# Kernel tuning notes

Measured on AMD Instinct MI355X. Metric: run time of the kernel, lower is better.

The kernel has to match this reference:

```python
import jax, jax.numpy as jnp
import numpy as np

N, E = 40000, 640000
DIN, C, EDIM = 128, 128, 32  # heads=1, out_channels=128

def setup_inputs() -> dict:
    key = jax.random.key(0)
    ks = jax.random.split(key, 9)
    x = jax.random.normal(ks[0], (N, DIN), dtype=jnp.float32)
    edge_index = jax.random.randint(ks[1], (2, E), 0, N, dtype=jnp.int64)
    edge_attr = jax.random.normal(ks[2], (E, EDIM), dtype=jnp.float32)
    s = 1.0 / np.sqrt(DIN)
    W = jax.random.normal(ks[3], (DIN, C), dtype=jnp.float32) * s
    W_edge = jax.random.normal(ks[4], (EDIM, C), dtype=jnp.float32) / np.sqrt(EDIM)
    att_src = jax.random.normal(ks[5], (C,), dtype=jnp.float32) * s
    att_dst = jax.random.normal(ks[6], (C,), dtype=jnp.float32) * s
    att_edge = jax.random.normal(ks[7], (C,), dtype=jnp.float32) * s
    bias = jnp.zeros((C,), dtype=jnp.float32)
    return {"x": x, "edge_index": edge_index, "edge_attr": edge_attr,
            "W": W, "W_edge": W_edge, "att_src": att_src, "att_dst": att_dst,
            "att_edge": att_edge, "bias": bias}

def reference(x, edge_index, edge_attr, W, W_edge, att_src, att_dst, att_edge, bias):
    # GATConv (heads=1) with edge features
    h = x @ W                      # [N, C] transformed node features
    a_src = h @ att_src            # [N] per-node source attention logits
    a_dst = h @ att_dst            # [N]
    src, dst = edge_index[0], edge_index[1]
    e = edge_attr @ W_edge         # [E, C]
    a_edge = e @ att_edge          # [E]
    alpha = a_src[src] + a_dst[dst] + a_edge            # [E]
    alpha = jax.nn.leaky_relu(alpha, negative_slope=0.2)
    # segment softmax over incoming edges of each destination node
    amax = jax.ops.segment_max(alpha, dst, num_segments=N)
    amax = jnp.where(jnp.isfinite(amax), amax, 0.0)     # empty segments -> -inf guard
    ex = jnp.exp(alpha - amax[dst])
    denom = jax.ops.segment_sum(ex, dst, num_segments=N)
    w = ex / (denom[dst] + 1e-16)                       # PyG softmax epsilon
    out = jax.ops.segment_sum(h[src] * w[:, None], dst, num_segments=N)  # [N, C]
    return out + bias
```

## Files before the change

kernel.cpp:

```cpp
#include <hip/hip_runtime.h>
#include <hip/hip_bf16.h>
#include <hip/hip_fp16.h>


#define DIN 128
#define CCH 128
#define EDIM 32
#define XS_LD 68

__device__ __forceinline__ unsigned pack_bf2(float a, float b) {
    __hip_bfloat16 x = __float2bfloat16(a);
    __hip_bfloat16 y = __float2bfloat16(b);
    unsigned short ux = *(unsigned short*)&x;
    unsigned short uy = *(unsigned short*)&y;
    return (unsigned)ux | ((unsigned)uy << 16);
}

__global__ __launch_bounds__(256) void gemm_h(
    const float* __restrict__ x, const float* __restrict__ W,
    const float* __restrict__ att_src, const float* __restrict__ att_dst,
    const int* __restrict__ ei, unsigned* __restrict__ hb,
    float* __restrict__ a_src, float* __restrict__ a_dst,
    int* __restrict__ count, int N, int E) {
    __shared__ float xs[64 * XS_LD];
    __shared__ float wl[64 * CCH];
    const int t = threadIdx.x;
    const int tx = t & 15;
    const int ty = t >> 4;
    const int row0 = blockIdx.x * 64;

    {
        const int* eid = ei + E;
        const int stride = gridDim.x * 256;
        for (int e = blockIdx.x * 256 + t; e < E; e += stride)
            atomicAdd(&count[eid[e]], 1);
    }

    float acc[4][8];
#pragma unroll
    for (int r = 0; r < 4; ++r)
#pragma unroll
        for (int c = 0; c < 8; ++c) acc[r][c] = 0.0f;

    for (int kh = 0; kh < 2; ++kh) {
        __syncthreads();
        {
            const float4* xg = (const float4*)x;
#pragma unroll
            for (int i = 0; i < 4; ++i) {
                int j4 = t + 256 * i;
                int r = j4 >> 4;
                int k = (j4 & 15) * 4;
                float4 v = xg[(size_t)(row0 + r) * 32 + kh * 16 + (j4 & 15)];
                *(float4*)&xs[r * XS_LD + k] = v;
            }
        }
        {
            const float4* wg = (const float4*)W;
#pragma unroll
            for (int i = 0; i < 8; ++i) {
                int j4 = t + 256 * i;
                int k = j4 >> 5;
                int c4 = j4 & 31;
                float4 v = wg[(size_t)(kh * 64 + k) * 32 + c4];
                *(float4*)&wl[k * CCH + c4 * 4] = v;
            }
        }
        __syncthreads();

#pragma unroll 4
        for (int k4 = 0; k4 < 64; k4 += 4) {
            float xr[4][4];
#pragma unroll
            for (int r = 0; r < 4; ++r) {
                float4 v = *(const float4*)&xs[(ty * 4 + r) * XS_LD + k4];
                xr[r][0] = v.x; xr[r][1] = v.y; xr[r][2] = v.z; xr[r][3] = v.w;
            }
            float wr[4][8];
#pragma unroll
            for (int i = 0; i < 4; ++i) {
                float4 w0 = *(const float4*)&wl[(k4 + i) * CCH + tx * 8];
                float4 w1 = *(const float4*)&wl[(k4 + i) * CCH + tx * 8 + 4];
                wr[i][0] = w0.x; wr[i][1] = w0.y; wr[i][2] = w0.z; wr[i][3] = w0.w;
                wr[i][4] = w1.x; wr[i][5] = w1.y; wr[i][6] = w1.z; wr[i][7] = w1.w;
            }
#pragma unroll
            for (int i = 0; i < 4; ++i)
#pragma unroll
                for (int r = 0; r < 4; ++r)
#pragma unroll
                    for (int c = 0; c < 8; ++c)
                        acc[r][c] += xr[r][i] * wr[i][c];
        }
    }

    float asv[8], adv[8];
#pragma unroll
    for (int c = 0; c < 8; ++c) {
        asv[c] = att_src[tx * 8 + c];
        adv[c] = att_dst[tx * 8 + c];
    }
#pragma unroll
    for (int r = 0; r < 4; ++r) {
        const int row = row0 + ty * 4 + r;
        unsigned u0 = pack_bf2(acc[r][0], acc[r][1]);
        unsigned u1 = pack_bf2(acc[r][2], acc[r][3]);
        unsigned u2 = pack_bf2(acc[r][4], acc[r][5]);
        unsigned u3 = pack_bf2(acc[r][6], acc[r][7]);
        *(uint4*)&hb[(size_t)row * 64 + tx * 4] = make_uint4(u0, u1, u2, u3);
        float ps = 0.0f, pd = 0.0f;
#pragma unroll
        for (int c = 0; c < 8; ++c) {
            ps += acc[r][c] * asv[c];
            pd += acc[r][c] * adv[c];
        }
        ps += __shfl_down(ps, 8, 16);
        pd += __shfl_down(pd, 8, 16);
        ps += __shfl_down(ps, 4, 16);
        pd += __shfl_down(pd, 4, 16);
        ps += __shfl_down(ps, 2, 16);
        pd += __shfl_down(pd, 2, 16);
        ps += __shfl_down(ps, 1, 16);
        pd += __shfl_down(pd, 1, 16);
        if (tx == 0) {
            a_src[row] = ps;
            a_dst[row] = pd;
        }
    }
}

__global__ __launch_bounds__(256) void scan_part(const int* __restrict__ count,
                                                 int* __restrict__ bsum, int N4) {
    int i4 = blockIdx.x * 256 + threadIdx.x;
    int s = 0;
    if (i4 < N4) {
        int4 vv = ((const int4*)count)[i4];
        s = vv.x + vv.y + vv.z + vv.w;
    }
#pragma unroll
    for (int off = 32; off; off >>= 1) s += __shfl_down(s, off);
    __shared__ int wsum[4];
    if ((threadIdx.x & 63) == 0) wsum[threadIdx.x >> 6] = s;
    __syncthreads();
    if (threadIdx.x == 0)
        bsum[blockIdx.x] = wsum[0] + wsum[1] + wsum[2] + wsum[3];
}

__global__ __launch_bounds__(256) void scan_apply(const int* __restrict__ count,
                                                  const int* __restrict__ bsum,
                                                  int* __restrict__ cursor,
                                                  int N4) {
    __shared__ int s_boff;
    __shared__ int wt[4];
    if (threadIdx.x == 0) {
        int s = 0;
        for (int i = 0; i < (int)blockIdx.x; ++i) s += bsum[i];
        s_boff = s;
    }
    int i4 = blockIdx.x * 256 + threadIdx.x;
    int4 vv = make_int4(0, 0, 0, 0);
    if (i4 < N4) vv = ((const int4*)count)[i4];
    int s = vv.x + vv.y + vv.z + vv.w;
    int lane = threadIdx.x & 63, w = threadIdx.x >> 6;
    int inc = s;
#pragma unroll
    for (int off = 1; off < 64; off <<= 1) {
        int u = __shfl_up(inc, off);
        if (lane >= off) inc += u;
    }
    if (lane == 63) wt[w] = inc;
    __syncthreads();
    int woff = 0;
    for (int i = 0; i < w; ++i) woff += wt[i];
    int exd = s_boff + woff + inc - s;
    if (i4 < N4) {
        int4 o;
        o.x = exd;
        o.y = exd + vv.x;
        o.z = exd + vv.x + vv.y;
        o.w = exd + vv.x + vv.y + vv.z;
        ((int4*)cursor)[i4] = o;
    }
}

__global__ __launch_bounds__(256) void edge_fill(
    const int* __restrict__ ei, const float* __restrict__ ea,
    const float* __restrict__ W_edge, const float* __restrict__ att_edge,
    const float* __restrict__ a_src, const float* __restrict__ a_dst,
    int* __restrict__ cursor, unsigned* __restrict__ pairs, int E) {
    __shared__ float vpart[8][EDIM];
    __shared__ float vl[EDIM];
    const int t = threadIdx.x;
    {
        int j = t & 31, seg = t >> 5;
        const float* wr = W_edge + j * CCH + seg * 16;
        const float* ar = att_edge + seg * 16;
        float p = 0.0f;
#pragma unroll
        for (int k = 0; k < 16; ++k) p += wr[k] * ar[k];
        vpart[seg][j] = p;
    }
    __syncthreads();
    if (t < EDIM) {
        float s = 0.0f;
#pragma unroll
        for (int i = 0; i < 8; ++i) s += vpart[i][t];
        vl[t] = s;
    }
    __syncthreads();

    int e = blockIdx.x * 256 + t;
    if (e >= E) return;
    const float4* ea4 = (const float4*)(ea + (size_t)e * EDIM);
    float s = 0.0f;
#pragma unroll
    for (int j = 0; j < 8; ++j) {
        float4 q = ea4[j];
        s += q.x * vl[4 * j] + q.y * vl[4 * j + 1] + q.z * vl[4 * j + 2] +
             q.w * vl[4 * j + 3];
    }
    int sn = ei[e];
    int dn = ei[E + e];
    float alpha = a_src[sn] + a_dst[dn] + s;
    alpha = alpha > 0.0f ? alpha : 0.2f * alpha;
    float ex = __expf(alpha);
    unsigned rec = (unsigned)(unsigned short)sn |
                   ((unsigned)__half_as_ushort(__float2half(ex)) << 16);
    int p = atomicAdd(&cursor[dn], 1);
    pairs[p] = rec;
}

#define GATHER_EDGE(rec)                                                      \
    {                                                                         \
        unsigned q = hb[(size_t)((rec) & 0xffffu) * 64 + lane];               \
        float exv = __half2float(__ushort_as_half((unsigned short)((rec) >> 16))); \
        a0 += exv * __uint_as_float(q << 16);                                 \
        a1 += exv * __uint_as_float(q & 0xffff0000u);                         \
        sum += exv;                                                           \
    }

__global__ __launch_bounds__(256) void gather_k(
    const int* __restrict__ count, const int* __restrict__ cursor,
    const unsigned* __restrict__ pairs, const unsigned* __restrict__ hb,
    const float* __restrict__ bias, float* __restrict__ out, int N) {
    int n = blockIdx.x * 4 + (threadIdx.x >> 6);
    int lane = threadIdx.x & 63;
    if (n >= N) return;
    int cnt = count[n];
    int start = cursor[n] - cnt;
    float a0 = 0.0f, a1 = 0.0f, sum = 0.0f;
    int j = 0;
    int head = (4 - (start & 3)) & 3;
    if (head > cnt) head = cnt;
    for (; j < head; ++j) {
        unsigned r = pairs[start + j];
        GATHER_EDGE(r);
    }
    int nq = (cnt - j) >> 2;
    if (nq > 0) {
        const uint4* pp4 = (const uint4*)(pairs + start + j);
        uint4 cur = pp4[0];
        for (int g = 0; g + 1 < nq; ++g) {
            uint4 nxt = pp4[g + 1];
            unsigned q0 = hb[(size_t)(cur.x & 0xffffu) * 64 + lane];
            unsigned q1 = hb[(size_t)(cur.y & 0xffffu) * 64 + lane];
            unsigned q2 = hb[(size_t)(cur.z & 0xffffu) * 64 + lane];
            unsigned q3 = hb[(size_t)(cur.w & 0xffffu) * 64 + lane];
            float e0 = __half2float(__ushort_as_half((unsigned short)(cur.x >> 16)));
            float e1 = __half2float(__ushort_as_half((unsigned short)(cur.y >> 16)));
            float e2 = __half2float(__ushort_as_half((unsigned short)(cur.z >> 16)));
            float e3 = __half2float(__ushort_as_half((unsigned short)(cur.w >> 16)));
            a0 += e0 * __uint_as_float(q0 << 16);
            a1 += e0 * __uint_as_float(q0 & 0xffff0000u);
            a0 += e1 * __uint_as_float(q1 << 16);
            a1 += e1 * __uint_as_float(q1 & 0xffff0000u);
            a0 += e2 * __uint_as_float(q2 << 16);
            a1 += e2 * __uint_as_float(q2 & 0xffff0000u);
            a0 += e3 * __uint_as_float(q3 << 16);
            a1 += e3 * __uint_as_float(q3 & 0xffff0000u);
            sum += (e0 + e1) + (e2 + e3);
            cur = nxt;
        }
        {
            unsigned q0 = hb[(size_t)(cur.x & 0xffffu) * 64 + lane];
            unsigned q1 = hb[(size_t)(cur.y & 0xffffu) * 64 + lane];
            unsigned q2 = hb[(size_t)(cur.z & 0xffffu) * 64 + lane];
            unsigned q3 = hb[(size_t)(cur.w & 0xffffu) * 64 + lane];
            float e0 = __half2float(__ushort_as_half((unsigned short)(cur.x >> 16)));
            float e1 = __half2float(__ushort_as_half((unsigned short)(cur.y >> 16)));
            float e2 = __half2float(__ushort_as_half((unsigned short)(cur.z >> 16)));
            float e3 = __half2float(__ushort_as_half((unsigned short)(cur.w >> 16)));
            a0 += e0 * __uint_as_float(q0 << 16);
            a1 += e0 * __uint_as_float(q0 & 0xffff0000u);
            a0 += e1 * __uint_as_float(q1 << 16);
            a1 += e1 * __uint_as_float(q1 & 0xffff0000u);
            a0 += e2 * __uint_as_float(q2 << 16);
            a1 += e2 * __uint_as_float(q2 & 0xffff0000u);
            a0 += e3 * __uint_as_float(q3 << 16);
            a1 += e3 * __uint_as_float(q3 & 0xffff0000u);
            sum += (e0 + e1) + (e2 + e3);
        }
        j += nq * 4;
    }
    for (; j < cnt; ++j) {
        unsigned r = pairs[start + j];
        GATHER_EDGE(r);
    }
    float inv = 1.0f / (sum + 1e-16f);
    float2 bv = *(const float2*)&bias[2 * lane];
    float2 o;
    o.x = a0 * inv + bv.x;
    o.y = a1 * inv + bv.y;
    *(float2*)&out[(size_t)n * CCH + 2 * lane] = o;
}

extern "C" void kernel_launch(void* const* d_in, const int* in_sizes, int n_in,
                              void* d_out, int out_size, void* d_ws, size_t ws_size,
                              hipStream_t stream) {
    const float* x        = (const float*)d_in[0];
    const int*   ei       = (const int*)d_in[1];
    const float* ea       = (const float*)d_in[2];
    const float* W        = (const float*)d_in[3];
    const float* W_edge   = (const float*)d_in[4];
    const float* att_src  = (const float*)d_in[5];
    const float* att_dst  = (const float*)d_in[6];
    const float* att_edge = (const float*)d_in[7];
    const float* bias     = (const float*)d_in[8];
    float* out = (float*)d_out;

    const int N = in_sizes[0] / DIN;
    const int E = in_sizes[2] / EDIM;
    const int N4 = N / 4;
    const int NB = (N4 + 255) / 256;

    char* ws = (char*)d_ws;
    unsigned* hb     = (unsigned*)ws;
    unsigned* pairs  = (unsigned*)(ws + (size_t)N * 64 * 4);
    float*    a_src  = (float*)(pairs + E);
    float*    a_dst  = a_src + N;
    int*      count  = (int*)(a_dst + N);
    int*      cursor = count + N;
    int*      bsum   = cursor + N;

    hipMemsetAsync(count, 0, (size_t)N * sizeof(int), stream);

    gemm_h<<<N / 64, 256, 0, stream>>>(x, W, att_src, att_dst, ei, hb,
                                       a_src, a_dst, count, N, E);
    scan_part<<<NB, 256, 0, stream>>>(count, bsum, N4);
    scan_apply<<<NB, 256, 0, stream>>>(count, bsum, cursor, N4);
    edge_fill<<<(E + 255) / 256, 256, 0, stream>>>(ei, ea, W_edge, att_edge,
                                                   a_src, a_dst, cursor, pairs, E);
    gather_k<<<(N + 3) / 4, 256, 0, stream>>>(count, cursor, pairs, hb, bias, out, N);
}
```

Before: 260.6 us.

## Record per-edge rank during counting to remove atomic cursor in edge fill

The counting atomics in gemm_h now return each edge's rank within its destination bucket, stored as a 16-bit value. edge_fill computes its output slot as offset plus rank instead of issuing a second atomicAdd on a cursor. a_dst and the offset are packed into one float2 per node so a single gather serves both. edge_fill also handles four edges per thread so independent loads can overlap. The cost is an extra E-sized rank write and read, and a rank that overflows if any in-degree exceeds 65535.

```diff
diff --git a/kernel.cpp b/kernel.cpp
--- a/kernel.cpp
+++ b/kernel.cpp
@@ -21,7 +21,8 @@
     const float* __restrict__ att_src, const float* __restrict__ att_dst,
     const int* __restrict__ ei, unsigned* __restrict__ hb,
     float* __restrict__ a_src, float* __restrict__ a_dst,
-    int* __restrict__ count, int N, int E) {
+    int* __restrict__ count, unsigned short* __restrict__ rank,
+    int N, int E) {
     __shared__ float xs[64 * XS_LD];
     __shared__ float wl[64 * CCH];
     const int t = threadIdx.x;
@@ -32,8 +33,10 @@
     {
         const int* eid = ei + E;
         const int stride = gridDim.x * 256;
-        for (int e = blockIdx.x * 256 + t; e < E; e += stride)
-            atomicAdd(&count[eid[e]], 1);
+        for (int e = blockIdx.x * 256 + t; e < E; e += stride) {
+            int r = atomicAdd(&count[eid[e]], 1);
+            rank[e] = (unsigned short)r;
+        }
     }
 
     float acc[4][8];
@@ -146,10 +149,10 @@
         bsum[blockIdx.x] = wsum[0] + wsum[1] + wsum[2] + wsum[3];
 }
 
-__global__ __launch_bounds__(256) void scan_apply(const int* __restrict__ count,
-                                                  const int* __restrict__ bsum,
-                                                  int* __restrict__ cursor,
-                                                  int N4) {
+__global__ __launch_bounds__(256) void scan_apply(
+    const int* __restrict__ count, const int* __restrict__ bsum,
+    const float* __restrict__ a_dst, int* __restrict__ offs,
+    float2* __restrict__ dinfo, int N4) {
     __shared__ int s_boff;
     __shared__ int wt[4];
     if (threadIdx.x == 0) {
@@ -179,15 +182,23 @@
         o.y = exd + vv.x;
         o.z = exd + vv.x + vv.y;
         o.w = exd + vv.x + vv.y + vv.z;
-        ((int4*)cursor)[i4] = o;
+        ((int4*)offs)[i4] = o;
+        float4 ad = ((const float4*)a_dst)[i4];
+        float4 d0 = make_float4(ad.x, __int_as_float(o.x),
+                                ad.y, __int_as_float(o.y));
+        float4 d1 = make_float4(ad.z, __int_as_float(o.z),
+                                ad.w, __int_as_float(o.w));
+        ((float4*)dinfo)[i4 * 2] = d0;
+        ((float4*)dinfo)[i4 * 2 + 1] = d1;
     }
 }
 
 __global__ __launch_bounds__(256) void edge_fill(
     const int* __restrict__ ei, const float* __restrict__ ea,
     const float* __restrict__ W_edge, const float* __restrict__ att_edge,
-    const float* __restrict__ a_src, const float* __restrict__ a_dst,
-    int* __restrict__ cursor, unsigned* __restrict__ pairs, int E) {
+    const float* __restrict__ a_src, const float2* __restrict__ dinfo,
+    const unsigned short* __restrict__ rank, unsigned* __restrict__ pairs,
+    int E) {
     __shared__ float vpart[8][EDIM];
     __shared__ float vl[EDIM];
     const int t = threadIdx.x;
@@ -209,25 +220,54 @@
     }
     __syncthreads();
 
-    int e = blockIdx.x * 256 + t;
-    if (e >= E) return;
-    const float4* ea4 = (const float4*)(ea + (size_t)e * EDIM);
-    float s = 0.0f;
-#pragma unroll
-    for (int j = 0; j < 8; ++j) {
-        float4 q = ea4[j];
-        s += q.x * vl[4 * j] + q.y * vl[4 * j + 1] + q.z * vl[4 * j + 2] +
-             q.w * vl[4 * j + 3];
-    }
-    int sn = ei[e];
-    int dn = ei[E + e];
-    float alpha = a_src[sn] + a_dst[dn] + s;
-    alpha = alpha > 0.0f ? alpha : 0.2f * alpha;
-    float ex = __expf(alpha);
-    unsigned rec = (unsigned)(unsigned short)sn |
-                   ((unsigned)__half_as_ushort(__float2half(ex)) << 16);
-    int p = atomicAdd(&cursor[dn], 1);
-    pairs[p] = rec;
+    const int base = blockIdx.x * 1024 + t;
+    int eidx[4], sn[4], dn[4], rk[4];
+    bool ok[4];
+#pragma unroll
+    for (int i = 0; i < 4; ++i) {
+        eidx[i] = base + 256 * i;
+        ok[i] = eidx[i] < E;
+    }
+#pragma unroll
+    for (int i = 0; i < 4; ++i) {
+        sn[i] = ok[i] ? ei[eidx[i]] : 0;
+        dn[i] = ok[i] ? ei[E + eidx[i]] : 0;
+    }
+#pragma unroll
+    for (int i = 0; i < 4; ++i) rk[i] = ok[i] ? (int)rank[eidx[i]] : 0;
+    float asv[4];
+    float2 di[4];
+#pragma unroll
+    for (int i = 0; i < 4; ++i) {
+        asv[i] = a_src[sn[i]];
+        di[i] = dinfo[dn[i]];
+    }
+    float dot[4];
+#pragma unroll
+    for (int i = 0; i < 4; ++i) {
+        float s = 0.0f;
+        if (ok[i]) {
+            const float4* ea4 = (const float4*)(ea + (size_t)eidx[i] * EDIM);
+#pragma unroll
+            for (int j = 0; j < 8; ++j) {
+                float4 q = ea4[j];
+                s += q.x * vl[4 * j] + q.y * vl[4 * j + 1] +
+                     q.z * vl[4 * j + 2] + q.w * vl[4 * j + 3];
+            }
+        }
+        dot[i] = s;
+    }
+#pragma unroll
+    for (int i = 0; i < 4; ++i) {
+        if (!ok[i]) continue;
+        float alpha = asv[i] + di[i].x + dot[i];
+        alpha = alpha > 0.0f ? alpha : 0.2f * alpha;
+        float ex = __expf(alpha);
+        unsigned rec = (unsigned)(unsigned short)sn[i] |
+                       ((unsigned)__half_as_ushort(__float2half(ex)) << 16);
+        int p = __float_as_int(di[i].y) + rk[i];
+        pairs[p] = rec;
+    }
 }
 
 #define GATHER_EDGE(rec)                                                      \
@@ -240,14 +280,14 @@
     }
 
 __global__ __launch_bounds__(256) void gather_k(
-    const int* __restrict__ count, const int* __restrict__ cursor,
+    const int* __restrict__ count, const int* __restrict__ offs,
     const unsigned* __restrict__ pairs, const unsigned* __restrict__ hb,
     const float* __restrict__ bias, float* __restrict__ out, int N) {
     int n = blockIdx.x * 4 + (threadIdx.x >> 6);
     int lane = threadIdx.x & 63;
     if (n >= N) return;
     int cnt = count[n];
-    int start = cursor[n] - cnt;
+    int start = offs[n];
     float a0 = 0.0f, a1 = 0.0f, sum = 0.0f;
     int j = 0;
     int head = (4 - (start & 3)) & 3;
@@ -334,21 +374,23 @@
     const int NB = (N4 + 255) / 256;
 
     char* ws = (char*)d_ws;
-    unsigned* hb     = (unsigned*)ws;
-    unsigned* pairs  = (unsigned*)(ws + (size_t)N * 64 * 4);
-    float*    a_src  = (float*)(pairs + E);
-    float*    a_dst  = a_src + N;
-    int*      count  = (int*)(a_dst + N);
-    int*      cursor = count + N;
-    int*      bsum   = cursor + N;
+    unsigned*       hb    = (unsigned*)ws;
+    unsigned*       pairs = (unsigned*)(ws + (size_t)N * 64 * 4);
+    unsigned short* rank  = (unsigned short*)(pairs + E);
+    float*  a_src = (float*)((char*)rank + (size_t)E * 2);
+    float*  a_dst = a_src + N;
+    float2* dinfo = (float2*)(a_dst + N);
+    int*    count = (int*)(dinfo + N);
+    int*    offs  = count + N;
+    int*    bsum  = offs + N;
 
     hipMemsetAsync(count, 0, (size_t)N * sizeof(int), stream);
 
     gemm_h<<<N / 64, 256, 0, stream>>>(x, W, att_src, att_dst, ei, hb,
-                                       a_src, a_dst, count, N, E);
+                                       a_src, a_dst, count, rank, N, E);
     scan_part<<<NB, 256, 0, stream>>>(count, bsum, N4);
-    scan_apply<<<NB, 256, 0, stream>>>(count, bsum, cursor, N4);
-    edge_fill<<<(E + 255) / 256, 256, 0, stream>>>(ei, ea, W_edge, att_edge,
-                                                   a_src, a_dst, cursor, pairs, E);
-    gather_k<<<(N + 3) / 4, 256, 0, stream>>>(count, cursor, pairs, hb, bias, out, N);
-}
+    scan_apply<<<NB, 256, 0, stream>>>(count, bsum, a_dst, offs, dinfo, N4);
+    edge_fill<<<(E + 1023) / 1024, 256, 0, stream>>>(ei, ea, W_edge, att_edge,
+                                                     a_src, dinfo, rank, pairs, E);
+    gather_k<<<(N + 3) / 4, 256, 0, stream>>>(count, offs, pairs, hb, bias, out, N);
+}
```

Result: no change. 256.0 us (-1.8%).
